# Kernel tuning notes

Measured on AMD Instinct MI355X. Metric: run time of the kernel, lower is better.

The kernel has to match this reference:

```python
import jax, jax.numpy as jnp
import numpy as np

B, N, H, V = 8192, 12, 512, 256  # batch, n_columns, hidden_size, per-column vocab
LN_EPS = 1e-5


def setup_inputs() -> dict:
    key = jax.random.key(0)
    k0, k1, k2, k3 = jax.random.split(key, 4)
    return {
        "input_embedding": jax.random.normal(k0, (B, H), dtype=jnp.float32),
        "features": jax.random.randint(k1, (B, N), 0, V),  # one categorical id per column
        "emb_tables": jax.random.normal(k2, (N, V, H), dtype=jnp.float32) * 0.02,
        "ln_gamma": jnp.ones((2 * H,), dtype=jnp.float32),
        "ln_beta": jnp.zeros((2 * H,), dtype=jnp.float32),
        "pred_W": jax.random.normal(k3, (N, 2 * H, V), dtype=jnp.float32) * 0.02,
        "pred_b": jnp.zeros((N, V), dtype=jnp.float32),
    }


def reference(input_embedding, features, emb_tables, ln_gamma, ln_beta, pred_W, pred_b):
    n = features.shape[1]
    # per-column embedding lookup: emb[b, n] = emb_tables[n, features[b, n]]  -> [B, N, H]
    emb = emb_tables[jnp.arange(n)[None, :], features]
    # _make_masked_sums: triu(diagonal=1) mask summed over dim 1 == exclusive prefix sum
    # over the column axis: masked_sums[b, j] = sum_{i < j} emb[b, i]
    masked_sums = jnp.cumsum(emb, axis=1) - emb  # [B, N, H]
    ctx = jnp.broadcast_to(input_embedding[:, None, :], emb.shape)  # [B, N, H]
    x = jnp.concatenate([ctx, masked_sums], axis=-1)  # [B, N, 2H]
    # LayerNorm over last dim, then exact (erf) GELU as in torch nn.GELU default
    mu = jnp.mean(x, axis=-1, keepdims=True)
    var = jnp.mean(jnp.square(x - mu), axis=-1, keepdims=True)
    xn = (x - mu) * jax.lax.rsqrt(var + LN_EPS) * ln_gamma + ln_beta
    act = jax.nn.gelu(xn, approximate=False)
    # per-column predictor heads: logits[b, n, :] = act[b, n, :] @ pred_W[n] + pred_b[n]
    logits = jnp.einsum('bnh,nhv->bnv', act, pred_W) + pred_b
    return logits
```

## Files before the change

### kernel.cpp

```cpp
#include <hip/hip_runtime.h>
#include <stdint.h>

#define B_SZ 8192
#define N_F 12
#define H_DIM 512
#define K_DIM 1024
#define V_DIM 256

typedef __attribute__((ext_vector_type(8))) __bf16 bf16x8;
typedef __attribute__((ext_vector_type(4))) float f32x4;

__device__ inline float gelu_f(float x) {
  float t = 1.5957691216057308f * x * (1.0f + 0.044715f * x * x);
  return x / (1.0f + __expf(-t));
}

__device__ inline void gld_lds16(const void* g, void* l) {
  __builtin_amdgcn_global_load_lds(
      (const __attribute__((address_space(1))) void*)g,
      (__attribute__((address_space(3))) void*)l, 16, 0, 0);
}

__global__ __launch_bounds__(256, 4) void k_prep(
    const float* __restrict__ ie, const int* __restrict__ feat,
    const float* __restrict__ tab, const float* __restrict__ gam,
    const float* __restrict__ bet, __bf16* __restrict__ act2) {
  const int lane = threadIdx.x & 63;
  const int b = blockIdx.x * 4 + (threadIdx.x >> 6);

  const float* cb = ie + (size_t)b * H_DIM + lane * 8;
  float4 c0 = *(const float4*)cb;
  float4 c1 = *(const float4*)(cb + 4);
  float s = c0.x + c0.y + c0.z + c0.w + c1.x + c1.y + c1.z + c1.w;
  float q = c0.x * c0.x + c0.y * c0.y + c0.z * c0.z + c0.w * c0.w +
            c1.x * c1.x + c1.y * c1.y + c1.z * c1.z + c1.w * c1.w;
#pragma unroll
  for (int o = 1; o < 64; o <<= 1) {
    s += __shfl_xor(s, o, 64);
    q += __shfl_xor(q, o, 64);
  }
  const float S1 = s, Q1 = q;

  const float4 gl0 = *(const float4*)(gam + lane * 8);
  const float4 gl1 = *(const float4*)(gam + lane * 8 + 4);
  const float4 el0 = *(const float4*)(bet + lane * 8);
  const float4 el1 = *(const float4*)(bet + lane * 8 + 4);
  const float4 g0 = *(const float4*)(gam + H_DIM + lane * 8);
  const float4 g1 = *(const float4*)(gam + H_DIM + lane * 8 + 4);
  const float4 e0 = *(const float4*)(bet + H_DIM + lane * 8);
  const float4 e1 = *(const float4*)(bet + H_DIM + lane * 8 + 4);

  float r[8];
#pragma unroll
  for (int i = 0; i < 8; ++i) r[i] = 0.f;

  const int sw = (lane & ~7) | ((lane & 7) ^ (b & 7));
  __bf16* arow = act2 + (size_t)b * K_DIM + sw * 8;

  for (int n = 0; n < N_F; ++n) {
    s = 0.f; q = 0.f;
#pragma unroll
    for (int i = 0; i < 8; ++i) { s += r[i]; q += r[i] * r[i]; }
#pragma unroll
    for (int o = 1; o < 64; o <<= 1) {
      s += __shfl_xor(s, o, 64);
      q += __shfl_xor(q, o, 64);
    }
    const float mean = (S1 + s) * (1.0f / 1024.0f);
    const float var = (Q1 + q) * (1.0f / 1024.0f) - mean * mean;
    const float rs = rsqrtf(var + 1e-5f);

    float4 t0, t1;
    const bool have = (n < N_F - 1);
    if (have) {
      const int f = feat[b * N_F + n];
      const float* tr = tab + ((size_t)n * V_DIM + f) * H_DIM + lane * 8;
      t0 = *(const float4*)tr;
      t1 = *(const float4*)(tr + 4);
    }

    bf16x8 pc;
    pc[0] = (__bf16)gelu_f((c0.x - mean) * rs * gl0.x + el0.x);
    pc[1] = (__bf16)gelu_f((c0.y - mean) * rs * gl0.y + el0.y);
    pc[2] = (__bf16)gelu_f((c0.z - mean) * rs * gl0.z + el0.z);
    pc[3] = (__bf16)gelu_f((c0.w - mean) * rs * gl0.w + el0.w);
    pc[4] = (__bf16)gelu_f((c1.x - mean) * rs * gl1.x + el1.x);
    pc[5] = (__bf16)gelu_f((c1.y - mean) * rs * gl1.y + el1.y);
    pc[6] = (__bf16)gelu_f((c1.z - mean) * rs * gl1.z + el1.z);
    pc[7] = (__bf16)gelu_f((c1.w - mean) * rs * gl1.w + el1.w);
    *(bf16x8*)(arow + (size_t)n * B_SZ * K_DIM) = pc;

    bf16x8 pk;
    pk[0] = (__bf16)gelu_f((r[0] - mean) * rs * g0.x + e0.x);
    pk[1] = (__bf16)gelu_f((r[1] - mean) * rs * g0.y + e0.y);
    pk[2] = (__bf16)gelu_f((r[2] - mean) * rs * g0.z + e0.z);
    pk[3] = (__bf16)gelu_f((r[3] - mean) * rs * g0.w + e0.w);
    pk[4] = (__bf16)gelu_f((r[4] - mean) * rs * g1.x + e1.x);
    pk[5] = (__bf16)gelu_f((r[5] - mean) * rs * g1.y + e1.y);
    pk[6] = (__bf16)gelu_f((r[6] - mean) * rs * g1.z + e1.z);
    pk[7] = (__bf16)gelu_f((r[7] - mean) * rs * g1.w + e1.w);
    *(bf16x8*)(arow + (size_t)n * B_SZ * K_DIM + H_DIM) = pk;

    if (have) {
      r[0] += t0.x; r[1] += t0.y; r[2] += t0.z; r[3] += t0.w;
      r[4] += t1.x; r[5] += t1.y; r[6] += t1.z; r[7] += t1.w;
    }
  }
}

__global__ __launch_bounds__(256) void k_wt(const float* __restrict__ W,
                                            __bf16* __restrict__ Wt) {
  __shared__ float tile[32][33];
  const int bid = blockIdx.x;
  const int n = bid >> 8;
  const int rem = bid & 255;
  const int kt = rem >> 3, vt = rem & 7;
  const int tx = threadIdx.x & 31, ty = threadIdx.x >> 5;
  const float* src = W + (size_t)n * K_DIM * V_DIM;
#pragma unroll
  for (int i = 0; i < 4; ++i) {
    const int k = kt * 32 + ty + i * 8;
    tile[ty + i * 8][tx] = src[(size_t)k * V_DIM + vt * 32 + tx];
  }
  __syncthreads();
  __bf16* dst = Wt + (size_t)n * V_DIM * K_DIM;
  const int t = threadIdx.x;
  if (t < 128) {
    const int v_l = t >> 2, c_l = t & 3;
    const int v = vt * 32 + v_l;
    bf16x8 pk;
#pragma unroll
    for (int e = 0; e < 8; ++e) pk[e] = (__bf16)tile[c_l * 8 + e][v_l];
    const int gc = kt * 4 + c_l;
    const int swc = (gc & ~7) | ((gc & 7) ^ (v & 7));
    *(bf16x8*)(dst + (size_t)v * K_DIM + swc * 8) = pk;
  }
}

__global__ __launch_bounds__(512, 4) void k_gemm(
    const __bf16* __restrict__ act2, const __bf16* __restrict__ Wt,
    const float* __restrict__ bias, float* __restrict__ out) {
  constexpr int BM = 128, BN = 256, BK = 64;
  __shared__ __align__(16) __bf16 As[BM * BK];
  __shared__ __align__(16) __bf16 Ws[BN * BK];

  const int n = blockIdx.y;
  const int b0 = blockIdx.x * BM;
  const int t = threadIdx.x;
  const int lane = t & 63;
  const int w = t >> 6;
  const int wm = w & 1;
  const int wn = w >> 1;
  const int l15 = lane & 15;
  const int lq = lane >> 4;

  f32x4 acc[4][4];
#pragma unroll
  for (int i = 0; i < 4; ++i)
#pragma unroll
    for (int j = 0; j < 4; ++j) acc[i][j] = (f32x4){0.f, 0.f, 0.f, 0.f};

  const __bf16* act2n = act2 + (size_t)n * B_SZ * K_DIM;
  const __bf16* Wtn = Wt + (size_t)n * V_DIM * K_DIM;

  const int lr8 = lane >> 3;
  const int lo8 = lane & 7;

  for (int kt = 0; kt < 16; ++kt) {
    const int k0 = kt * BK;
    __syncthreads();
#pragma unroll
    for (int p = 0; p < 4; ++p) {
      const int v0 = w * 32 + p * 8;
      gld_lds16(Wtn + (size_t)(v0 + lr8) * K_DIM + k0 + lo8 * 8, Ws + v0 * BK);
    }
#pragma unroll
    for (int p = 0; p < 2; ++p) {
      const int r0 = w * 16 + p * 8;
      gld_lds16(act2n + (size_t)(b0 + r0 + lr8) * K_DIM + k0 + lo8 * 8,
                As + r0 * BK);
    }
    __syncthreads();
#pragma unroll
    for (int ks = 0; ks < 2; ++ks) {
      const int cs = ks * 4 + lq;
      bf16x8 af[4], bb[4];
#pragma unroll
      for (int i = 0; i < 4; ++i) {
        const int row = wm * 64 + i * 16 + l15;
        af[i] = *(const bf16x8*)(As + row * BK + ((cs ^ (row & 7)) << 3));
      }
#pragma unroll
      for (int j = 0; j < 4; ++j) {
        const int row = wn * 64 + j * 16 + l15;
        bb[j] = *(const bf16x8*)(Ws + row * BK + ((cs ^ (row & 7)) << 3));
      }
#pragma unroll
      for (int i = 0; i < 4; ++i)
#pragma unroll
        for (int j = 0; j < 4; ++j)
          acc[i][j] =
              __builtin_amdgcn_mfma_f32_16x16x32_bf16(af[i], bb[j], acc[i][j], 0, 0, 0);
    }
  }

#pragma unroll
  for (int j = 0; j < 4; ++j) {
    const int v = wn * 64 + j * 16 + l15;
    const float bv = bias[n * V_DIM + v];
#pragma unroll
    for (int i = 0; i < 4; ++i) {
      const int rb = wm * 64 + i * 16 + lq * 4;
#pragma unroll
      for (int r = 0; r < 4; ++r) {
        out[((size_t)(b0 + rb + r) * N_F + n) * V_DIM + v] = acc[i][j][r] + bv;
      }
    }
  }
}

extern "C" void kernel_launch(void* const* d_in, const int* in_sizes, int n_in,
                              void* d_out, int out_size, void* d_ws, size_t ws_size,
                              hipStream_t stream) {
  const float* ie = (const float*)d_in[0];
  const int* feat = (const int*)d_in[1];
  const float* tab = (const float*)d_in[2];
  const float* gam = (const float*)d_in[3];
  const float* bet = (const float*)d_in[4];
  const float* predW = (const float*)d_in[5];
  const float* predb = (const float*)d_in[6];
  float* out = (float*)d_out;

  char* ws = (char*)d_ws;
  __bf16* act2 = (__bf16*)ws;
  __bf16* Wt = (__bf16*)(ws + 201326592);

  hipLaunchKernelGGL(k_prep, dim3(B_SZ / 4), dim3(256), 0, stream, ie, feat,
                     tab, gam, bet, act2);
  hipLaunchKernelGGL(k_wt, dim3(3072), dim3(256), 0, stream, predW, Wt);
  hipLaunchKernelGGL(k_gemm, dim3(B_SZ / 128, N_F), dim3(512), 0, stream,
                     act2, Wt, predb, out);
}
```

Measured before the change: 286.1 us.

## Triple-buffer GEMM LDS tiles with async global-to-LDS prefetch pipeline

```diff
diff --git a/kernel.cpp b/kernel.cpp
--- a/kernel.cpp
+++ b/kernel.cpp
@@ -137,12 +137,12 @@
   }
 }
 
-__global__ __launch_bounds__(512, 4) void k_gemm(
+__global__ __launch_bounds__(512, 2) void k_gemm(
     const __bf16* __restrict__ act2, const __bf16* __restrict__ Wt,
     const float* __restrict__ bias, float* __restrict__ out) {
   constexpr int BM = 128, BN = 256, BK = 64;
-  __shared__ __align__(16) __bf16 As[BM * BK];
-  __shared__ __align__(16) __bf16 Ws[BN * BK];
+  __shared__ __align__(16) __bf16 As[3][BM * BK];
+  __shared__ __align__(16) __bf16 Ws[3][BN * BK];
 
   const int n = blockIdx.y;
   const int b0 = blockIdx.x * BM;
@@ -153,34 +153,36 @@
   const int wn = w >> 1;
   const int l15 = lane & 15;
   const int lq = lane >> 4;
-
-  f32x4 acc[4][4];
-#pragma unroll
-  for (int i = 0; i < 4; ++i)
-#pragma unroll
-    for (int j = 0; j < 4; ++j) acc[i][j] = (f32x4){0.f, 0.f, 0.f, 0.f};
+  const int lr8 = lane >> 3;
+  const int lo8 = lane & 7;
 
   const __bf16* act2n = act2 + (size_t)n * B_SZ * K_DIM;
   const __bf16* Wtn = Wt + (size_t)n * V_DIM * K_DIM;
 
-  const int lr8 = lane >> 3;
-  const int lo8 = lane & 7;
-
-  for (int kt = 0; kt < 16; ++kt) {
+  f32x4 acc[4][4];
+#pragma unroll
+  for (int i = 0; i < 4; ++i)
+#pragma unroll
+    for (int j = 0; j < 4; ++j) acc[i][j] = (f32x4){0.f, 0.f, 0.f, 0.f};
+
+  auto stage = [&](int buf, int kt) {
     const int k0 = kt * BK;
-    __syncthreads();
 #pragma unroll
     for (int p = 0; p < 4; ++p) {
       const int v0 = w * 32 + p * 8;
-      gld_lds16(Wtn + (size_t)(v0 + lr8) * K_DIM + k0 + lo8 * 8, Ws + v0 * BK);
+      gld_lds16(Wtn + (size_t)(v0 + lr8) * K_DIM + k0 + lo8 * 8,
+                &Ws[buf][v0 * BK]);
     }
 #pragma unroll
     for (int p = 0; p < 2; ++p) {
       const int r0 = w * 16 + p * 8;
       gld_lds16(act2n + (size_t)(b0 + r0 + lr8) * K_DIM + k0 + lo8 * 8,
-                As + r0 * BK);
-    }
-    __syncthreads();
+                &As[buf][r0 * BK]);
+    }
+  };
+
+  auto compute = [&](int buf) {
+    __builtin_amdgcn_s_setprio(1);
 #pragma unroll
     for (int ks = 0; ks < 2; ++ks) {
       const int cs = ks * 4 + lq;
@@ -188,21 +190,42 @@
 #pragma unroll
       for (int i = 0; i < 4; ++i) {
         const int row = wm * 64 + i * 16 + l15;
-        af[i] = *(const bf16x8*)(As + row * BK + ((cs ^ (row & 7)) << 3));
+        af[i] = *(const bf16x8*)(&As[buf][row * BK + ((cs ^ (row & 7)) << 3)]);
       }
 #pragma unroll
       for (int j = 0; j < 4; ++j) {
         const int row = wn * 64 + j * 16 + l15;
-        bb[j] = *(const bf16x8*)(Ws + row * BK + ((cs ^ (row & 7)) << 3));
+        bb[j] = *(const bf16x8*)(&Ws[buf][row * BK + ((cs ^ (row & 7)) << 3)]);
       }
 #pragma unroll
       for (int i = 0; i < 4; ++i)
 #pragma unroll
         for (int j = 0; j < 4; ++j)
-          acc[i][j] =
-              __builtin_amdgcn_mfma_f32_16x16x32_bf16(af[i], bb[j], acc[i][j], 0, 0, 0);
-    }
-  }
+          acc[i][j] = __builtin_amdgcn_mfma_f32_16x16x32_bf16(af[i], bb[j],
+                                                              acc[i][j], 0, 0, 0);
+    }
+    __builtin_amdgcn_s_setprio(0);
+  };
+
+  stage(0, 0);
+  stage(1, 1);
+
+#pragma unroll
+  for (int kt = 0; kt < 14; ++kt) {
+    asm volatile("s_waitcnt vmcnt(6)" ::: "memory");
+    __builtin_amdgcn_s_barrier();
+    asm volatile("" ::: "memory");
+    stage((kt + 2) % 3, kt + 2);
+    compute(kt % 3);
+  }
+  asm volatile("s_waitcnt vmcnt(6)" ::: "memory");
+  __builtin_amdgcn_s_barrier();
+  asm volatile("" ::: "memory");
+  compute(14 % 3);
+  asm volatile("s_waitcnt vmcnt(0)" ::: "memory");
+  __builtin_amdgcn_s_barrier();
+  asm volatile("" ::: "memory");
+  compute(15 % 3);
 
 #pragma unroll
   for (int j = 0; j < 4; ++j) {
```

After: 300.9 us. 5.2% more time.

## Store activations row-major per batch, alias output buffer, shrink GEMM tile

Applied to the files above, without the earlier changes.

```diff
diff --git a/kernel.cpp b/kernel.cpp
--- a/kernel.cpp
+++ b/kernel.cpp
@@ -24,7 +24,7 @@
 __global__ __launch_bounds__(256, 4) void k_prep(
     const float* __restrict__ ie, const int* __restrict__ feat,
     const float* __restrict__ tab, const float* __restrict__ gam,
-    const float* __restrict__ bet, __bf16* __restrict__ act2) {
+    const float* __restrict__ bet, __bf16* actA, __bf16* __restrict__ ctx2) {
   const int lane = threadIdx.x & 63;
   const int b = blockIdx.x * 4 + (threadIdx.x >> 6);
 
@@ -55,7 +55,8 @@
   for (int i = 0; i < 8; ++i) r[i] = 0.f;
 
   const int sw = (lane & ~7) | ((lane & 7) ^ (b & 7));
-  __bf16* arow = act2 + (size_t)b * K_DIM + sw * 8;
+  __bf16* arowM = actA + (size_t)b * N_F * H_DIM + sw * 8;
+  __bf16* arowC = ctx2 + (size_t)b * N_F * H_DIM + sw * 8;
 
   for (int n = 0; n < N_F; ++n) {
     s = 0.f; q = 0.f;
@@ -88,7 +89,7 @@
     pc[5] = (__bf16)gelu_f((c1.y - mean) * rs * gl1.y + el1.y);
     pc[6] = (__bf16)gelu_f((c1.z - mean) * rs * gl1.z + el1.z);
     pc[7] = (__bf16)gelu_f((c1.w - mean) * rs * gl1.w + el1.w);
-    *(bf16x8*)(arow + (size_t)n * B_SZ * K_DIM) = pc;
+    *(bf16x8*)(arowC + (size_t)n * H_DIM) = pc;
 
     bf16x8 pk;
     pk[0] = (__bf16)gelu_f((r[0] - mean) * rs * g0.x + e0.x);
@@ -99,7 +100,7 @@
     pk[5] = (__bf16)gelu_f((r[5] - mean) * rs * g1.y + e1.y);
     pk[6] = (__bf16)gelu_f((r[6] - mean) * rs * g1.z + e1.z);
     pk[7] = (__bf16)gelu_f((r[7] - mean) * rs * g1.w + e1.w);
-    *(bf16x8*)(arow + (size_t)n * B_SZ * K_DIM + H_DIM) = pk;
+    *(bf16x8*)(arowM + (size_t)n * H_DIM) = pk;
 
     if (have) {
       r[0] += t0.x; r[1] += t0.y; r[2] += t0.z; r[3] += t0.w;
@@ -137,10 +138,11 @@
   }
 }
 
-__global__ __launch_bounds__(512, 4) void k_gemm(
-    const __bf16* __restrict__ act2, const __bf16* __restrict__ Wt,
-    const float* __restrict__ bias, float* __restrict__ out) {
-  constexpr int BM = 128, BN = 256, BK = 64;
+__global__ __launch_bounds__(256, 3) void k_gemm(
+    const __bf16* __restrict__ ctx2, const __bf16* actA,
+    const __bf16* __restrict__ Wt, const float* __restrict__ bias,
+    float* out) {
+  constexpr int BM = 64, BN = 256, BK = 64;
   __shared__ __align__(16) __bf16 As[BM * BK];
   __shared__ __align__(16) __bf16 Ws[BN * BK];
 
@@ -149,36 +151,46 @@
   const int t = threadIdx.x;
   const int lane = t & 63;
   const int w = t >> 6;
-  const int wm = w & 1;
-  const int wn = w >> 1;
   const int l15 = lane & 15;
   const int lq = lane >> 4;
-
-  f32x4 acc[4][4];
-#pragma unroll
-  for (int i = 0; i < 4; ++i)
-#pragma unroll
-    for (int j = 0; j < 4; ++j) acc[i][j] = (f32x4){0.f, 0.f, 0.f, 0.f};
-
-  const __bf16* act2n = act2 + (size_t)n * B_SZ * K_DIM;
-  const __bf16* Wtn = Wt + (size_t)n * V_DIM * K_DIM;
-
   const int lr8 = lane >> 3;
   const int lo8 = lane & 7;
 
+  const __bf16* Wtn = Wt + (size_t)n * V_DIM * K_DIM;
+
+  f32x4 acc[4][4];
+#pragma unroll
+  for (int i = 0; i < 4; ++i)
+#pragma unroll
+    for (int j = 0; j < 4; ++j) acc[i][j] = (f32x4){0.f, 0.f, 0.f, 0.f};
+
+#pragma unroll
   for (int kt = 0; kt < 16; ++kt) {
-    const int k0 = kt * BK;
     __syncthreads();
 #pragma unroll
     for (int p = 0; p < 4; ++p) {
-      const int v0 = w * 32 + p * 8;
-      gld_lds16(Wtn + (size_t)(v0 + lr8) * K_DIM + k0 + lo8 * 8, Ws + v0 * BK);
-    }
-#pragma unroll
-    for (int p = 0; p < 2; ++p) {
-      const int r0 = w * 16 + p * 8;
-      gld_lds16(act2n + (size_t)(b0 + r0 + lr8) * K_DIM + k0 + lo8 * 8,
-                As + r0 * BK);
+      const int v0 = w * 64 + p * 16 + (lr8 & 8);
+      (void)v0;
+    }
+#pragma unroll
+    for (int p = 0; p < 8; p += 2) {
+      const int r0 = w * 64 + p * 8;
+      gld_lds16(Wtn + (size_t)(r0 + lr8) * K_DIM + kt * BK + lo8 * 8,
+                Ws + r0 * BK);
+      const int r1 = w * 64 + (p + 1) * 8;
+      gld_lds16(Wtn + (size_t)(r1 + lr8) * K_DIM + kt * BK + lo8 * 8,
+                Ws + r1 * BK);
+    }
+    {
+      const __bf16* src = (kt < 8) ? ctx2 : actA;
+      const int kc = (kt < 8) ? kt * 64 : (kt - 8) * 64;
+#pragma unroll
+      for (int p = 0; p < 2; ++p) {
+        const int r0 = w * 16 + p * 8;
+        gld_lds16(src + ((size_t)(b0 + r0 + lr8) * N_F + n) * H_DIM + kc +
+                      lo8 * 8,
+                  As + r0 * BK);
+      }
     }
     __syncthreads();
 #pragma unroll
@@ -187,30 +199,30 @@
       bf16x8 af[4], bb[4];
 #pragma unroll
       for (int i = 0; i < 4; ++i) {
-        const int row = wm * 64 + i * 16 + l15;
+        const int row = i * 16 + l15;
         af[i] = *(const bf16x8*)(As + row * BK + ((cs ^ (row & 7)) << 3));
       }
 #pragma unroll
       for (int j = 0; j < 4; ++j) {
-        const int row = wn * 64 + j * 16 + l15;
+        const int row = w * 64 + j * 16 + l15;
         bb[j] = *(const bf16x8*)(Ws + row * BK + ((cs ^ (row & 7)) << 3));
       }
 #pragma unroll
       for (int i = 0; i < 4; ++i)
 #pragma unroll
         for (int j = 0; j < 4; ++j)
-          acc[i][j] =
-              __builtin_amdgcn_mfma_f32_16x16x32_bf16(af[i], bb[j], acc[i][j], 0, 0, 0);
+          acc[i][j] = __builtin_amdgcn_mfma_f32_16x16x32_bf16(af[i], bb[j],
+                                                              acc[i][j], 0, 0, 0);
     }
   }
 
 #pragma unroll
   for (int j = 0; j < 4; ++j) {
-    const int v = wn * 64 + j * 16 + l15;
+    const int v = w * 64 + j * 16 + l15;
     const float bv = bias[n * V_DIM + v];
 #pragma unroll
     for (int i = 0; i < 4; ++i) {
-      const int rb = wm * 64 + i * 16 + lq * 4;
+      const int rb = i * 16 + lq * 4;
 #pragma unroll
       for (int r = 0; r < 4; ++r) {
         out[((size_t)(b0 + rb + r) * N_F + n) * V_DIM + v] = acc[i][j][r] + bv;
@@ -231,13 +243,15 @@
   const float* predb = (const float*)d_in[6];
   float* out = (float*)d_out;
 
+  __bf16* actA = (__bf16*)d_out;
+
   char* ws = (char*)d_ws;
-  __bf16* act2 = (__bf16*)ws;
-  __bf16* Wt = (__bf16*)(ws + 201326592);
+  __bf16* ctx2 = (__bf16*)ws;
+  __bf16* Wt = (__bf16*)(ws + 100663296);
 
   hipLaunchKernelGGL(k_prep, dim3(B_SZ / 4), dim3(256), 0, stream, ie, feat,
-                     tab, gam, bet, act2);
+                     tab, gam, bet, actA, ctx2);
   hipLaunchKernelGGL(k_wt, dim3(3072), dim3(256), 0, stream, predW, Wt);
-  hipLaunchKernelGGL(k_gemm, dim3(B_SZ / 128, N_F), dim3(512), 0, stream,
-                     act2, Wt, predb, out);
-}
+  hipLaunchKernelGGL(k_gemm, dim3(B_SZ / 64, N_F), dim3(256), 0, stream,
+                     ctx2, actA, Wt, predb, out);
+}
```

Result: faster. 262.3 us (-8.3%).
